# Optimization experiments

Measured on AMD Instinct MI355X. Metric: run time of the kernel, lower is better.

Reference implementation:

```python
import jax, jax.numpy as jnp
import numpy as np

B, H, W, DIM = 2, 64, 64, 128
NH = 4
HD = DIM // NH
KS = 7
DIL = 2
SCALE = HD ** -0.5


def _natten_idx(L, k, dil):
    """Per-position neighborhood start + rpb start (NATTEN semantics), as gather index tables."""
    ns = k // 2
    starts = np.empty(L, np.int32)
    pbs = np.empty(L, np.int32)
    for i in range(L):
        if dil <= 1:
            s = max(i - ns, 0) + (i + ns >= L) * (L - i - ns - 1)
            p = ns + (i < ns) * (ns - i) + (i + ns >= L) * (L - i - 1 - ns)
        else:
            if i - ns * dil < 0:
                s = i % dil
                p = k - 1 - (i // dil)
            elif i + ns * dil >= L:
                imodd = i % dil
                a = (L // dil) * dil
                b = L - a
                if imodd < b:
                    s = L - b + imodd - 2 * ns * dil
                else:
                    s = a + imodd - k * dil
                p = (L - i - 1) // dil
            else:
                s = i - ns * dil
                p = ns
        starts[i] = s
        pbs[i] = p
    key_idx = starts[:, None] + dil * np.arange(k, dtype=np.int32)  # [L, k] key positions
    pb_idx = pbs[:, None] + np.arange(k, dtype=np.int32)            # [L, k] rpb positions
    return key_idx, pb_idx


def setup_inputs() -> dict:
    key = jax.random.key(0)
    ks = jax.random.split(key, 12)
    shp = (B, H, W, DIM)
    q = jax.random.normal(ks[0], shp, jnp.float32)
    k = jax.random.normal(ks[1], shp, jnp.float32)
    v = jax.random.normal(ks[2], shp, jnp.float32)
    def lin(kk):
        return jax.random.normal(kk, (DIM, DIM), jnp.float32) * (DIM ** -0.5)
    Wq, Wk, Wv, Wo = lin(ks[3]), lin(ks[4]), lin(ks[5]), lin(ks[6])
    bq = jnp.zeros((DIM,), jnp.float32)
    bk = jnp.zeros((DIM,), jnp.float32)
    bv = jnp.zeros((DIM,), jnp.float32)
    bo = jnp.zeros((DIM,), jnp.float32)
    rpb = jax.random.normal(ks[7], (NH, 2 * KS - 1, 2 * KS - 1), jnp.float32) * 0.02
    return {"q": q, "k": k, "v": v, "Wq": Wq, "bq": bq, "Wk": Wk, "bk": bk,
            "Wv": Wv, "bv": bv, "rpb": rpb, "Wo": Wo, "bo": bo}


def _forward(q, k, v, Wq, bq, Wk, bk, Wv, bv, rpb, Wo, bo):
    Bc, Hc, Wc, C = q.shape
    ii, pi = _natten_idx(Hc, KS, DIL)   # [H, K]
    jj, pj = _natten_idx(Wc, KS, DIL)   # [W, K]

    def heads(x, Wm, bm):
        # [B,H,W,C] -> [B,NH,H,W,HD]
        return (x @ Wm + bm).reshape(Bc, Hc, Wc, NH, HD).transpose(0, 3, 1, 2, 4)

    qh = heads(q, Wq, bq) * SCALE
    kh = heads(k, Wk, bk)
    vh = heads(v, Wv, bv)

    # Gather KxK dilated neighborhoods: [B,NH,H,K,W,K,HD]
    knbr = kh[:, :, ii][:, :, :, :, jj]
    vnbr = vh[:, :, ii][:, :, :, :, jj]

    # attention logits per pixel over its KxK neighborhood: [B,NH,H,W,K,K]
    attn = jnp.einsum('bnhwd,bnhkwld->bnhwkl', qh, knbr)
    # relative position bias lookup: [NH,H,K,W,K] -> [NH,H,W,K,K]
    bias = rpb[:, pi][:, :, :, pj].transpose(0, 1, 3, 2, 4)
    attn = attn + bias[None]

    attn = jax.nn.softmax(attn.reshape(Bc, NH, Hc, Wc, KS * KS), axis=-1)
    attn = attn.reshape(Bc, NH, Hc, Wc, KS, KS)

    out = jnp.einsum('bnhwkl,bnhkwld->bnhwd', attn, vnbr)
    out = out.transpose(0, 2, 3, 1, 4).reshape(Bc, Hc, Wc, C)
    return out @ Wo + bo


def reference(q, k, v, Wq, bq, Wk, bk, Wv, bv, rpb, Wo, bo):
    return _forward(q, k, v, Wq, bq, Wk, bk, Wv, bv, rpb, Wo, bo)
```

## Files before the change

### kernel.cpp

```cpp
#include <hip/hip_runtime.h>
#include <hip/hip_bf16.h>
#include <math.h>

#define BB 2
#define HH 64
#define WW 64
#define DIMC 128
#define NH 4
#define HD 32
#define KS 7
#define DIL 2
#define NPIX (BB * HH * WW)
#define SCALE 0.17677669529663687f

typedef short bf16x8 __attribute__((ext_vector_type(8)));
typedef float f32x4  __attribute__((ext_vector_type(4)));

__device__ __forceinline__ short bf16r(float f) {
    union { float f; unsigned u; } x; x.f = f;
    unsigned r = x.u + 0x7FFF + ((x.u >> 16) & 1);
    return (short)(r >> 16);
}
__device__ __forceinline__ float uasf(unsigned u) {
    union { unsigned u; float f; } x; x.u = u; return x.f;
}

__global__ __launch_bounds__(256) void prep_w(
    const float* __restrict__ Wq, const float* __restrict__ Wk,
    const float* __restrict__ Wv, const float* __restrict__ Wo,
    short* __restrict__ Wt)
{
    const int z  = blockIdx.x >> 2;
    const int ks = blockIdx.x & 3;
    const float* W = (z == 0) ? Wq : (z == 1) ? Wk : (z == 2) ? Wv : Wo;

    __shared__ short T[32][136];
    const int t = threadIdx.x;
    const float4* Wg = (const float4*)(W + ks * 32 * 128);

    float4 xv[4];
#pragma unroll
    for (int u = 0; u < 4; ++u) xv[u] = Wg[u * 256 + t];
#pragma unroll
    for (int u = 0; u < 4; ++u) {
        const int e = u * 256 + t;
        const int r = e >> 5;
        const int c = (e & 31) * 4;
        short4 s4;
        s4.x = bf16r(xv[u].x); s4.y = bf16r(xv[u].y);
        s4.z = bf16r(xv[u].z); s4.w = bf16r(xv[u].w);
        *(short4*)&T[r][c] = s4;
    }
    __syncthreads();

    const int c = t >> 1;
    const int h = (t & 1) * 16;
    bf16x8 lo, hi;
#pragma unroll
    for (int i = 0; i < 8; ++i) { lo[i] = T[h + i][c]; hi[i] = T[h + 8 + i][c]; }
    short* outp = Wt + z * 16384 + c * 128 + ks * 32 + h;
    *(bf16x8*)(outp)     = lo;
    *(bf16x8*)(outp + 8) = hi;
}

__global__ __launch_bounds__(256) void qkv_mfma(
    const float* __restrict__ q, const float* __restrict__ k,
    const float* __restrict__ v, const short* __restrict__ Wt,
    const float* __restrict__ bq, const float* __restrict__ bk,
    const float* __restrict__ bv,
    float* __restrict__ qh, short* __restrict__ khb, short* __restrict__ vhb)
{
    const int z = blockIdx.y;
    const float* X    = (z == 0) ? q  : (z == 1) ? k  : v;
    const float* bias = (z == 0) ? bq : (z == 1) ? bk : bv;
    const short* Wz   = Wt + z * 16384;

    const int t    = threadIdx.x;
    const int wv   = t >> 6;
    const int lane = t & 63;
    const int lr   = lane & 15;
    const int lg   = lane >> 4;
    const int row0 = blockIdx.x * 32 + (wv & 1) * 16;
    const int col0 = (wv >> 1) * 64;

    bf16x8 bfr[16];
#pragma unroll
    for (int nt = 0; nt < 4; ++nt) {
        const short* wrow = Wz + (col0 + nt * 16 + lr) * 128 + lg * 8;
#pragma unroll
        for (int kk = 0; kk < 4; ++kk)
            bfr[nt * 4 + kk] = *(const bf16x8*)(wrow + kk * 32);
    }

    const float* xrow = X + (size_t)(row0 + lr) * 128 + lg * 8;
    bf16x8 a[4];
#pragma unroll
    for (int kk = 0; kk < 4; ++kk) {
        const float4 x0 = *(const float4*)(xrow + kk * 32);
        const float4 x1 = *(const float4*)(xrow + kk * 32 + 4);
        bf16x8 av;
        av[0] = bf16r(x0.x); av[1] = bf16r(x0.y);
        av[2] = bf16r(x0.z); av[3] = bf16r(x0.w);
        av[4] = bf16r(x1.x); av[5] = bf16r(x1.y);
        av[6] = bf16r(x1.z); av[7] = bf16r(x1.w);
        a[kk] = av;
    }

#pragma unroll
    for (int nt = 0; nt < 4; ++nt) {
        const int col = col0 + nt * 16 + lr;
        f32x4 acc = {0.f, 0.f, 0.f, 0.f};
#pragma unroll
        for (int kk = 0; kk < 4; ++kk)
            acc = __builtin_amdgcn_mfma_f32_16x16x32_bf16(a[kk], bfr[nt * 4 + kk], acc, 0, 0, 0);
        const float bc = bias[col];
        if (z == 0) {
#pragma unroll
            for (int jj = 0; jj < 4; ++jj)
                qh[(size_t)(row0 + lg * 4 + jj) * 128 + col] = (acc[jj] + bc) * SCALE;
        } else {
            short* Yb = (z == 1) ? khb : vhb;
#pragma unroll
            for (int jj = 0; jj < 4; ++jj)
                Yb[(size_t)(row0 + lg * 4 + jj) * 128 + col] = bf16r(acc[jj] + bc);
        }
    }
}

__device__ __forceinline__ void natten_idx(int i, int& s, int& p)
{
    if (i < 6) {
        s = i & 1;
        p = 6 - (i >> 1);
    } else if (i >= 58) {
        s = 50 + (i & 1);
        p = (63 - i) >> 1;
    } else {
        s = i - 6;
        p = 3;
    }
}

__global__ __launch_bounds__(512) void natten_out(
    const float* __restrict__ qh, const short* __restrict__ khb,
    const short* __restrict__ vhb, const float* __restrict__ rpb,
    const short* __restrict__ Wt, const float* __restrict__ bo,
    float* __restrict__ out)
{
    __shared__ short attS[16][136];

    const int blk  = blockIdx.x;
    const int work = (blk & 7) * 64 + (blk >> 3);
    const int t    = threadIdx.x;

    {
        const int lane4 = t & 3;
        const int n   = (t >> 2) & 3;
        const int kih = (t >> 4) & 1;
        const int p   = t >> 5;
        const int g   = work * 16 + p;
        const int j   = g & 63;
        const int i   = (g >> 6) & 63;
        const int b   = g >> 12;

        int si, pi0, sj, pj0;
        natten_idx(i, si, pi0);
        natten_idx(j, sj, pj0);

        const int coff = n * 32 + lane4 * 8;
        const size_t pixb = (size_t)(b * 4096 + i * 64 + j);
        const float4 q0 = *(const float4*)(qh + pixb * 128 + coff);
        const float4 q1 = *(const float4*)(qh + pixb * 128 + coff + 4);

        const float* rp = rpb + n * 169;

        float m = -1e30f, l = 0.0f;
        float o[8] = {0.f, 0.f, 0.f, 0.f, 0.f, 0.f, 0.f, 0.f};

#pragma unroll
        for (int r = 0; r < 4; ++r) {
            const int ki  = kih * 4 + r;
            const int kic = (ki > 6) ? 6 : ki;
            const bool masked = (ki == 7);
            const int iy = si + 2 * kic;
            const size_t rowbase = ((size_t)(b * 4096 + iy * 64)) * 128 + coff;
            const float* rrow = rp + (pi0 + kic) * 13 + pj0;

            float d[7];
#pragma unroll
            for (int kj = 0; kj < 7; ++kj) {
                const int ix = sj + 2 * kj;
                const uint4 kv = *(const uint4*)(khb + rowbase + (size_t)ix * 128);
                float dd =      q0.x * uasf(kv.x << 16);
                dd = fmaf(q0.y, uasf(kv.x & 0xFFFF0000u), dd);
                dd = fmaf(q0.z, uasf(kv.y << 16), dd);
                dd = fmaf(q0.w, uasf(kv.y & 0xFFFF0000u), dd);
                dd = fmaf(q1.x, uasf(kv.z << 16), dd);
                dd = fmaf(q1.y, uasf(kv.z & 0xFFFF0000u), dd);
                dd = fmaf(q1.z, uasf(kv.w << 16), dd);
                dd = fmaf(q1.w, uasf(kv.w & 0xFFFF0000u), dd);
                d[kj] = dd;
            }
#pragma unroll
            for (int kj = 0; kj < 7; ++kj) d[kj] += __shfl_xor(d[kj], 1);
#pragma unroll
            for (int kj = 0; kj < 7; ++kj) d[kj] += __shfl_xor(d[kj], 2);
#pragma unroll
            for (int kj = 0; kj < 7; ++kj)
                d[kj] = masked ? -1e30f : (d[kj] + rrow[kj]);

            const float g01 = fmaxf(d[0], d[1]);
            const float g23 = fmaxf(d[2], d[3]);
            const float g45 = fmaxf(d[4], d[5]);
            const float gm  = fmaxf(fmaxf(g01, g23), fmaxf(g45, d[6]));
            const float mn  = fmaxf(m, gm);
            const float corr = __expf(m - mn);
            m = mn;
            l *= corr;
#pragma unroll
            for (int e = 0; e < 8; ++e) o[e] *= corr;

#pragma unroll
            for (int kj = 0; kj < 7; ++kj) {
                const float pe = __expf(d[kj] - m);
                d[kj] = pe;
                l += pe;
            }

#pragma unroll
            for (int kj = 0; kj < 7; ++kj) {
                const int ix = sj + 2 * kj;
                const uint4 vv = *(const uint4*)(vhb + rowbase + (size_t)ix * 128);
                const float pe = d[kj];
                o[0] = fmaf(pe, uasf(vv.x << 16),          o[0]);
                o[1] = fmaf(pe, uasf(vv.x & 0xFFFF0000u),  o[1]);
                o[2] = fmaf(pe, uasf(vv.y << 16),          o[2]);
                o[3] = fmaf(pe, uasf(vv.y & 0xFFFF0000u),  o[3]);
                o[4] = fmaf(pe, uasf(vv.z << 16),          o[4]);
                o[5] = fmaf(pe, uasf(vv.z & 0xFFFF0000u),  o[5]);
                o[6] = fmaf(pe, uasf(vv.w << 16),          o[6]);
                o[7] = fmaf(pe, uasf(vv.w & 0xFFFF0000u),  o[7]);
            }
        }

        const float mo  = __shfl_xor(m, 16);
        const float lo_ = __shfl_xor(l, 16);
        const float mm  = fmaxf(m, mo);
        const float f   = __expf(m - mm);
        const float fo  = __expf(mo - mm);
        float lm = l * f + lo_ * fo;
#pragma unroll
        for (int e = 0; e < 8; ++e) {
            const float oo = __shfl_xor(o[e], 16);
            o[e] = o[e] * f + oo * fo;
        }

        const float inv = 1.0f / lm;
        if (kih == 0) {
            bf16x8 ow;
#pragma unroll
            for (int e = 0; e < 8; ++e) ow[e] = bf16r(o[e] * inv);
            *(bf16x8*)&attS[p][coff] = ow;
        }
    }

    __syncthreads();

    {
        const int wv   = t >> 6;
        const int lane = t & 63;
        const int lr   = lane & 15;
        const int lg   = lane >> 4;
        const int col0 = wv * 16;
        const short* Wz = Wt + 3 * 16384;

        bf16x8 bfr[4];
        const short* wrow = Wz + (col0 + lr) * 128 + lg * 8;
#pragma unroll
        for (int kk = 0; kk < 4; ++kk)
            bfr[kk] = *(const bf16x8*)(wrow + kk * 32);

        bf16x8 a[4];
#pragma unroll
        for (int kk = 0; kk < 4; ++kk)
            a[kk] = *(const bf16x8*)&attS[lr][kk * 32 + lg * 8];

        f32x4 acc = {0.f, 0.f, 0.f, 0.f};
#pragma unroll
        for (int kk = 0; kk < 4; ++kk)
            acc = __builtin_amdgcn_mfma_f32_16x16x32_bf16(a[kk], bfr[kk], acc, 0, 0, 0);

        const int col = col0 + lr;
        const float bc = bo[col];
#pragma unroll
        for (int jj = 0; jj < 4; ++jj)
            out[(size_t)(work * 16 + lg * 4 + jj) * 128 + col] = acc[jj] + bc;
    }
}

extern "C" void kernel_launch(void* const* d_in, const int* in_sizes, int n_in,
                              void* d_out, int out_size, void* d_ws, size_t ws_size,
                              hipStream_t stream)
{
    const float* q   = (const float*)d_in[0];
    const float* k   = (const float*)d_in[1];
    const float* v   = (const float*)d_in[2];
    const float* Wq  = (const float*)d_in[3];
    const float* bq  = (const float*)d_in[4];
    const float* Wk  = (const float*)d_in[5];
    const float* bk  = (const float*)d_in[6];
    const float* Wv  = (const float*)d_in[7];
    const float* bv  = (const float*)d_in[8];
    const float* rpb = (const float*)d_in[9];
    const float* Wo  = (const float*)d_in[10];
    const float* bo  = (const float*)d_in[11];

    float* ws   = (float*)d_ws;
    float* qh   = ws;
    short* khb  = (short*)(ws + (size_t)NPIX * 128);
    short* vhb  = khb + (size_t)NPIX * 128;
    short* Wt   = vhb + (size_t)NPIX * 128;
    float* out  = (float*)d_out;

    hipLaunchKernelGGL(prep_w, dim3(16), dim3(256), 0, stream, Wq, Wk, Wv, Wo, Wt);

    hipLaunchKernelGGL(qkv_mfma, dim3(256, 3), dim3(256), 0, stream,
                       q, k, v, Wt, bq, bk, bv, qh, khb, vhb);

    hipLaunchKernelGGL(natten_out, dim3(512), dim3(512), 0, stream,
                       qh, khb, vhb, rpb, Wt, bo, out);
}
```

Before: 40.55 us.

## Split head dim across 8 lanes instead of splitting kernel rows across lane halves

Remaps the 32 threads per pixel so that 8 lanes each own 4 channels of a head and loop over all 7 kernel rows. Previously 4 lanes owned 8 channels each and the two halves took 4 rows apiece, one of them padded with a masked dummy row. The new mapping drops that wasted eighth row and the final cross-half softmax merge. In exchange each lane does twice as many serial row iterations, adds a third shuffle stage per dot product, and issues narrower 8-byte loads.

New measurement: 40.77 us. About the same (+0.6%).

```diff
diff --git a/kernel.cpp b/kernel.cpp
--- a/kernel.cpp
+++ b/kernel.cpp
@@ -154,9 +154,8 @@
     const int t    = threadIdx.x;
 
     {
-        const int lane4 = t & 3;
-        const int n   = (t >> 2) & 3;
-        const int kih = (t >> 4) & 1;
+        const int lane8 = t & 7;
+        const int n   = (t >> 3) & 3;
         const int p   = t >> 5;
         const int g   = work * 16 + p;
         const int j   = g & 63;
@@ -167,38 +166,30 @@
         natten_idx(i, si, pi0);
         natten_idx(j, sj, pj0);
 
-        const int coff = n * 32 + lane4 * 8;
+        const int coff = n * 32 + lane8 * 4;
         const size_t pixb = (size_t)(b * 4096 + i * 64 + j);
-        const float4 q0 = *(const float4*)(qh + pixb * 128 + coff);
-        const float4 q1 = *(const float4*)(qh + pixb * 128 + coff + 4);
+        const float4 qv = *(const float4*)(qh + pixb * 128 + coff);
 
         const float* rp = rpb + n * 169;
 
         float m = -1e30f, l = 0.0f;
-        float o[8] = {0.f, 0.f, 0.f, 0.f, 0.f, 0.f, 0.f, 0.f};
-
-#pragma unroll
-        for (int r = 0; r < 4; ++r) {
-            const int ki  = kih * 4 + r;
-            const int kic = (ki > 6) ? 6 : ki;
-            const bool masked = (ki == 7);
-            const int iy = si + 2 * kic;
+        float o0 = 0.f, o1 = 0.f, o2 = 0.f, o3 = 0.f;
+
+#pragma unroll
+        for (int ki = 0; ki < 7; ++ki) {
+            const int iy = si + 2 * ki;
             const size_t rowbase = ((size_t)(b * 4096 + iy * 64)) * 128 + coff;
-            const float* rrow = rp + (pi0 + kic) * 13 + pj0;
+            const float* rrow = rp + (pi0 + ki) * 13 + pj0;
 
             float d[7];
 #pragma unroll
             for (int kj = 0; kj < 7; ++kj) {
                 const int ix = sj + 2 * kj;
-                const uint4 kv = *(const uint4*)(khb + rowbase + (size_t)ix * 128);
-                float dd =      q0.x * uasf(kv.x << 16);
-                dd = fmaf(q0.y, uasf(kv.x & 0xFFFF0000u), dd);
-                dd = fmaf(q0.z, uasf(kv.y << 16), dd);
-                dd = fmaf(q0.w, uasf(kv.y & 0xFFFF0000u), dd);
-                dd = fmaf(q1.x, uasf(kv.z << 16), dd);
-                dd = fmaf(q1.y, uasf(kv.z & 0xFFFF0000u), dd);
-                dd = fmaf(q1.z, uasf(kv.w << 16), dd);
-                dd = fmaf(q1.w, uasf(kv.w & 0xFFFF0000u), dd);
+                const uint2 kv = *(const uint2*)(khb + rowbase + (size_t)ix * 128);
+                float dd =      qv.x * uasf(kv.x << 16);
+                dd = fmaf(qv.y, uasf(kv.x & 0xFFFF0000u), dd);
+                dd = fmaf(qv.z, uasf(kv.y << 16), dd);
+                dd = fmaf(qv.w, uasf(kv.y & 0xFFFF0000u), dd);
                 d[kj] = dd;
             }
 #pragma unroll
@@ -206,8 +197,9 @@
 #pragma unroll
             for (int kj = 0; kj < 7; ++kj) d[kj] += __shfl_xor(d[kj], 2);
 #pragma unroll
-            for (int kj = 0; kj < 7; ++kj)
-                d[kj] = masked ? -1e30f : (d[kj] + rrow[kj]);
+            for (int kj = 0; kj < 7; ++kj) d[kj] += __shfl_xor(d[kj], 4);
+#pragma unroll
+            for (int kj = 0; kj < 7; ++kj) d[kj] += rrow[kj];
 
             const float g01 = fmaxf(d[0], d[1]);
             const float g23 = fmaxf(d[2], d[3]);
@@ -217,8 +209,7 @@
             const float corr = __expf(m - mn);
             m = mn;
             l *= corr;
-#pragma unroll
-            for (int e = 0; e < 8; ++e) o[e] *= corr;
+            o0 *= corr; o1 *= corr; o2 *= corr; o3 *= corr;
 
 #pragma unroll
             for (int kj = 0; kj < 7; ++kj) {
@@ -230,38 +221,22 @@
 #pragma unroll
             for (int kj = 0; kj < 7; ++kj) {
                 const int ix = sj + 2 * kj;
-                const uint4 vv = *(const uint4*)(vhb + rowbase + (size_t)ix * 128);
+                const uint2 vv = *(const uint2*)(vhb + rowbase + (size_t)ix * 128);
                 const float pe = d[kj];
-                o[0] = fmaf(pe, uasf(vv.x << 16),          o[0]);
-                o[1] = fmaf(pe, uasf(vv.x & 0xFFFF0000u),  o[1]);
-                o[2] = fmaf(pe, uasf(vv.y << 16),          o[2]);
-                o[3] = fmaf(pe, uasf(vv.y & 0xFFFF0000u),  o[3]);
-                o[4] = fmaf(pe, uasf(vv.z << 16),          o[4]);
-                o[5] = fmaf(pe, uasf(vv.z & 0xFFFF0000u),  o[5]);
-                o[6] = fmaf(pe, uasf(vv.w << 16),          o[6]);
-                o[7] = fmaf(pe, uasf(vv.w & 0xFFFF0000u),  o[7]);
+                o0 = fmaf(pe, uasf(vv.x << 16),          o0);
+                o1 = fmaf(pe, uasf(vv.x & 0xFFFF0000u),  o1);
+                o2 = fmaf(pe, uasf(vv.y << 16),          o2);
+                o3 = fmaf(pe, uasf(vv.y & 0xFFFF0000u),  o3);
             }
         }
 
-        const float mo  = __shfl_xor(m, 16);
-        const float lo_ = __shfl_xor(l, 16);
-        const float mm  = fmaxf(m, mo);
-        const float f   = __expf(m - mm);
-        const float fo  = __expf(mo - mm);
-        float lm = l * f + lo_ * fo;
-#pragma unroll
-        for (int e = 0; e < 8; ++e) {
-            const float oo = __shfl_xor(o[e], 16);
-            o[e] = o[e] * f + oo * fo;
-        }
-
-        const float inv = 1.0f / lm;
-        if (kih == 0) {
-            bf16x8 ow;
-#pragma unroll
-            for (int e = 0; e < 8; ++e) ow[e] = bf16r(o[e] * inv);
-            *(bf16x8*)&attS[p][coff] = ow;
-        }
+        const float inv = 1.0f / l;
+        short4 ow;
+        ow.x = bf16r(o0 * inv);
+        ow.y = bf16r(o1 * inv);
+        ow.z = bf16r(o2 * inv);
+        ow.w = bf16r(o3 * inv);
+        *(short4*)&attS[p][coff] = ow;
     }
 
     __syncthreads();
```
